# Kernel tuning notes

Hardware: AMD Instinct MI355X
Metric: run time of the kernel (lower is better)

The kernel has to match this reference:

```python
import jax, jax.numpy as jnp
import numpy as np


def setup_inputs() -> dict:
    key = jax.random.key(0)
    k1, k2, k3 = jax.random.split(key, 3)
    B, A, F, OUT = 4, 200, 128, 128
    scalar_features = jax.random.normal(k1, (B, A, F), dtype=jnp.float32)
    distances = jax.random.normal(k2, (B, A, A, 3), dtype=jnp.float32)
    # Xavier-uniform-like init for weight (in_feats=2F, out_feats=OUT)
    limit = float(np.sqrt(6.0 / (2 * F + OUT)))
    weight = jax.random.uniform(k3, (2 * F, OUT), dtype=jnp.float32,
                                minval=-limit, maxval=limit)
    bias = jnp.zeros((OUT,), dtype=jnp.float32)
    return {"scalar_features": scalar_features, "distances": distances,
            "weight": weight, "bias": bias}


def reference(scalar_features, distances, weight, bias):
    # scalar_features: [B, A, F]; distances: [B, A, A, C] (C=3)
    # weight: [2F, OUT]; bias: [OUT]
    B, A, F = scalar_features.shape
    OUT = weight.shape[1]
    # Pairwise concat via two half-GEMMs (equivalent to concat([x_i, x_j]) @ W):
    # concat(x_i, x_j) @ W = x_i @ W[:F] + x_j @ W[F:]
    h_i = jnp.einsum('baf,fo->bao', scalar_features, weight[:F])   # [B, A, OUT]
    h_j = jnp.einsum('baf,fo->bao', scalar_features, weight[F:])   # [B, A, OUT]
    pair = h_i[:, :, None, :] + h_j[:, None, :, :] + bias          # [B, A, A, OUT]
    # Broadcast-multiply with distances: [B, A, A, C, OUT]
    vector_features = pair[:, :, :, None, :] * distances[..., None]
    return vector_features
```

## Files before the change

kernel.cpp:

```cpp
#include <hip/hip_runtime.h>

typedef float f32x4 __attribute__((ext_vector_type(4)));

#define B_DIM   4
#define A_DIM   200
#define F_DIM   128
#define OUT_DIM 128
#define NROW    (B_DIM * A_DIM)
#define HJ_OFF  (NROW * (OUT_DIM / 4))
#define JRC     40
#define JRW     10

__global__ void __launch_bounds__(256) gemm_h_kernel(
    const float* __restrict__ x,
    const float* __restrict__ W,
    const float* __restrict__ bias,
    float* __restrict__ h)
{
    const int row  = blockIdx.x;
    const int t    = threadIdx.x;
    const int o    = t & 127;
    const int half = t >> 7;
    __shared__ float xs[F_DIM];
    if (t < F_DIM) xs[t] = x[row * F_DIM + t];
    __syncthreads();

    const float* __restrict__ Wh = W + half * F_DIM * OUT_DIM;
    float acc = 0.f;
#pragma unroll
    for (int f = 0; f < F_DIM; ++f)
        acc = fmaf(xs[f], Wh[f * OUT_DIM + o], acc);

    if (half == 0) h[row * OUT_DIM + o]          = acc + bias[o];
    else           h[(NROW + row) * OUT_DIM + o] = acc;
}

__global__ void __launch_bounds__(256) expand_kernel(
    const f32x4* __restrict__ h4,
    const float* __restrict__ dist,
    f32x4* __restrict__ out)
{
    const unsigned t     = threadIdx.x;
    const unsigned l     = t & 63u;
    const unsigned wv    = t >> 6;
    const unsigned o4    = l & 31u;
    const unsigned jlh   = l >> 5;
    const unsigned jrow0 = blockIdx.x * JRC;

    const unsigned birow = jrow0 / 200u;
    const unsigned j0    = jrow0 - birow * 200u;
    const unsigned b     = birow / 200u;

    const unsigned wrow  = jrow0 + wv * JRW;
    const f32x4 hi = h4[birow * 32u + o4];

    f32x4 p[5];
    float d[5][3];
#pragma unroll
    for (int k = 0; k < 5; ++k) {
        const unsigned r = 2u * k + jlh;
        const f32x4 hj = h4[HJ_OFF + (b * 200u + j0 + wv * JRW + r) * 32u + o4];
        p[k] = hi + hj;
        d[k][0] = dist[(wrow + r) * 3u + 0u];
        d[k][1] = dist[(wrow + r) * 3u + 1u];
        d[k][2] = dist[(wrow + r) * 3u + 2u];
    }

    f32x4* __restrict__ obase = out + (unsigned long long)wrow * 96ull;
#pragma unroll
    for (int k = 0; k < 5; ++k) {
        const unsigned rbase = (2u * k + jlh) * 96u + o4;
        obase[rbase +  0u] = p[k] * d[k][0];
        obase[rbase + 32u] = p[k] * d[k][1];
        obase[rbase + 64u] = p[k] * d[k][2];
    }
}

extern "C" void kernel_launch(void* const* d_in, const int* in_sizes, int n_in,
                              void* d_out, int out_size, void* d_ws, size_t ws_size,
                              hipStream_t stream) {
    const float* x    = (const float*)d_in[0];
    const float* dist = (const float*)d_in[1];
    const float* W    = (const float*)d_in[2];
    const float* bias = (const float*)d_in[3];

    float* h = (float*)d_ws;

    gemm_h_kernel<<<NROW, 256, 0, stream>>>(x, W, bias, h);

    expand_kernel<<<160000 / JRC, 256, 0, stream>>>((const f32x4*)h, dist,
                                                    (f32x4*)d_out);
}
```

Measured before the change: 48.83 us.

## Make expand kernel persistent with double-buffered unit loads and stores

The expand kernel now launches a quarter as many waves, and each wave processes four 10-row units strided across the grid. It alternates two register buffers so the loads for the next unit are issued before the stores of the current one. The goal is to overlap load latency with the store stream and reduce launch and wave-scheduling overhead. In exchange it uses more registers and has fewer waves in flight to hide memory latency.

```diff
diff --git a/kernel.cpp b/kernel.cpp
--- a/kernel.cpp
+++ b/kernel.cpp
@@ -8,8 +8,9 @@
 #define OUT_DIM 128
 #define NROW    (B_DIM * A_DIM)
 #define HJ_OFF  (NROW * (OUT_DIM / 4))
-#define JRC     40
 #define JRW     10
+#define NWAVES  4000
+#define NUNITS  (160000 / JRW)
 
 __global__ void __launch_bounds__(256) gemm_h_kernel(
     const float* __restrict__ x,
@@ -35,45 +36,69 @@
     else           h[(NROW + row) * OUT_DIM + o] = acc;
 }
 
+struct Unit {
+    f32x4 hi;
+    f32x4 hj[5];
+    float d[5][3];
+    unsigned wrow;
+};
+
+__device__ __forceinline__ void load_unit(unsigned unit, unsigned o4, unsigned jlh,
+                                          const f32x4* __restrict__ h4,
+                                          const float* __restrict__ dist,
+                                          Unit& U)
+{
+    const unsigned jrow0 = unit * JRW;
+    const unsigned birow = jrow0 / 200u;
+    const unsigned j0    = jrow0 - birow * 200u;
+    const unsigned b     = birow / 200u;
+    U.wrow = jrow0;
+    U.hi   = h4[birow * 32u + o4];
+#pragma unroll
+    for (int k = 0; k < 5; ++k) {
+        const unsigned r = 2u * k + jlh;
+        U.hj[k]   = h4[HJ_OFF + (b * 200u + j0 + r) * 32u + o4];
+        U.d[k][0] = dist[(jrow0 + r) * 3u + 0u];
+        U.d[k][1] = dist[(jrow0 + r) * 3u + 1u];
+        U.d[k][2] = dist[(jrow0 + r) * 3u + 2u];
+    }
+}
+
+__device__ __forceinline__ void store_unit(const Unit& U, unsigned o4, unsigned jlh,
+                                           f32x4* __restrict__ out)
+{
+    f32x4* __restrict__ obase = out + (unsigned long long)U.wrow * 96ull;
+#pragma unroll
+    for (int k = 0; k < 5; ++k) {
+        const f32x4 p = U.hi + U.hj[k];
+        const unsigned rbase = (2u * k + jlh) * 96u + o4;
+        obase[rbase +  0u] = p * U.d[k][0];
+        obase[rbase + 32u] = p * U.d[k][1];
+        obase[rbase + 64u] = p * U.d[k][2];
+    }
+}
+
 __global__ void __launch_bounds__(256) expand_kernel(
     const f32x4* __restrict__ h4,
     const float* __restrict__ dist,
     f32x4* __restrict__ out)
 {
-    const unsigned t     = threadIdx.x;
-    const unsigned l     = t & 63u;
-    const unsigned wv    = t >> 6;
-    const unsigned o4    = l & 31u;
-    const unsigned jlh   = l >> 5;
-    const unsigned jrow0 = blockIdx.x * JRC;
+    const unsigned t   = threadIdx.x;
+    const unsigned l   = t & 63u;
+    const unsigned wv  = t >> 6;
+    const unsigned o4  = l & 31u;
+    const unsigned jlh = l >> 5;
+    const unsigned wid = blockIdx.x * 4u + wv;
 
-    const unsigned birow = jrow0 / 200u;
-    const unsigned j0    = jrow0 - birow * 200u;
-    const unsigned b     = birow / 200u;
-
-    const unsigned wrow  = jrow0 + wv * JRW;
-    const f32x4 hi = h4[birow * 32u + o4];
-
-    f32x4 p[5];
-    float d[5][3];
-#pragma unroll
-    for (int k = 0; k < 5; ++k) {
-        const unsigned r = 2u * k + jlh;
-        const f32x4 hj = h4[HJ_OFF + (b * 200u + j0 + wv * JRW + r) * 32u + o4];
-        p[k] = hi + hj;
-        d[k][0] = dist[(wrow + r) * 3u + 0u];
-        d[k][1] = dist[(wrow + r) * 3u + 1u];
-        d[k][2] = dist[(wrow + r) * 3u + 2u];
-    }
-
-    f32x4* __restrict__ obase = out + (unsigned long long)wrow * 96ull;
-#pragma unroll
-    for (int k = 0; k < 5; ++k) {
-        const unsigned rbase = (2u * k + jlh) * 96u + o4;
-        obase[rbase +  0u] = p[k] * d[k][0];
-        obase[rbase + 32u] = p[k] * d[k][1];
-        obase[rbase + 64u] = p[k] * d[k][2];
-    }
+    Unit A, B;
+    load_unit(wid,                o4, jlh, h4, dist, A);
+    load_unit(wid + NWAVES,       o4, jlh, h4, dist, B);
+    store_unit(A, o4, jlh, out);
+    load_unit(wid + 2u * NWAVES,  o4, jlh, h4, dist, A);
+    store_unit(B, o4, jlh, out);
+    load_unit(wid + 3u * NWAVES,  o4, jlh, h4, dist, B);
+    store_unit(A, o4, jlh, out);
+    store_unit(B, o4, jlh, out);
 }
 
 extern "C" void kernel_launch(void* const* d_in, const int* in_sizes, int n_in,
@@ -88,6 +113,6 @@
 
     gemm_h_kernel<<<NROW, 256, 0, stream>>>(x, W, bias, h);
 
-    expand_kernel<<<160000 / JRC, 256, 0, stream>>>((const f32x4*)h, dist,
-                                                    (f32x4*)d_out);
+    expand_kernel<<<NWAVES / 4, 256, 0, stream>>>((const f32x4*)h, dist,
+                                                  (f32x4*)d_out);
 }
```

Measured after the change: 50.00 us. 1.02x slower.
